# Kernel optimization log

Measured on AMD Instinct MI355X. Metric: run time of the kernel, lower is better.

## Reference

```python
import jax, jax.numpy as jnp
import numpy as np

H = W = 256
CX = CY = 128
N_RINGS = 16
RING_W = 8


def _ring_indices():
    """Static per-ring pixel coordinate lists (cv2 filled-circle rasterization
    approximated by Euclidean distance: ring i = { inner_r < dist <= outer_r }).
    Ring 0 excludes the exact center pixel, matching cv2.circle(radius=0) erase."""
    yy, xx = np.mgrid[0:H, 0:W]
    dist = np.sqrt((xx - CX) ** 2 + (yy - CY) ** 2)
    rings = []
    for i in range(N_RINGS):
        m = (dist <= (i + 1) * RING_W) & (dist > i * RING_W)
        ys, xs = np.nonzero(m)
        rings.append((jnp.asarray(ys), jnp.asarray(xs)))
    return rings

_RINGS = _ring_indices()


def setup_inputs() -> dict:
    key = jax.random.key(0)
    # normalized image in [0,1) so denorm->uint8 quantization never wraps
    image_tensor = jax.random.uniform(key, (256, 3, 256, 256), dtype=jnp.float32)
    return {"image_tensor": image_tensor}


def reference(image_tensor):
    # denormalize and quantize exactly like (img*0.5+0.5)*255 -> uint8 (truncation)
    img = jnp.floor((image_tensor * 0.5 + 0.5) * 255.0)  # [B,3,H,W], values 0..255
    feats = []
    for ys, xs in _RINGS:  # fixed 16-iteration structural loop
        px = img[:, :, ys, xs]                # [B, 3, N_ring] gather
        mean = jnp.mean(px, axis=-1)          # [B, 3]
        std = jnp.std(px, axis=-1)            # population std (ddof=0) like np
        med = jnp.median(px, axis=-1)         # [B, 3]
        feats.append(jnp.concatenate([mean, std, med], axis=-1))  # [B, 9]
    return jnp.stack(feats, axis=1)  # [B, 16, 9]
```

## Files before the change

kernel.cpp:

```cpp
#include <hip/hip_runtime.h>

#define IH 256
#define IW 256
#define NRINGS 16
#define LUT_WORDS (IH * IW / 4)

__global__ __launch_bounds__(256)
void k_ringlut(unsigned int* __restrict__ lut) {
    const int gid = blockIdx.x * 256 + threadIdx.x;
    const int y   = gid >> 6;
    const int x0  = (gid & 63) * 4;
    const int dy  = y - 128;
    const int dy2 = dy * dy;
    unsigned int w = 0;
    #pragma unroll
    for (int j = 0; j < 4; ++j) {
        const int dx = x0 + j - 128;
        const int d2 = dy2 + dx * dx;
        unsigned int r;
        if (d2 == 0 || d2 > 16384) r = 255u;
        else {
            int kk = (int)ceilf(sqrtf((float)d2) * 0.125f);
            if (64 * kk * kk < d2) kk++;
            else if (kk > 1 && 64 * (kk - 1) * (kk - 1) >= d2) kk--;
            r = (unsigned)(kk - 1);
        }
        w |= r << (8 * j);
    }
    lut[gid] = w;
}

__global__ __launch_bounds__(1024)
void radial_fused(const float* __restrict__ img,
                  const unsigned int* __restrict__ lut,
                  float* __restrict__ out) {
    const int b   = blockIdx.x;
    const int tid = threadIdx.x;

    __shared__ unsigned int hist[NRINGS * 3 * 256];

    for (int i = tid; i < NRINGS * 3 * 256; i += 1024) hist[i] = 0u;
    __syncthreads();

    const int xg = (tid & 63) * 4;
    const int r0 = tid >> 6;
    const float* base = img + (size_t)b * 3 * IH * IW;
    const int lc = xg >> 2;

    unsigned int rw[16];
    #pragma unroll
    for (int k = 0; k < 16; ++k) {
        const int y = r0 + (k << 4);
        rw[k] = lut[(y << 6) + lc];
    }

    #pragma unroll
    for (int k = 0; k < 16; ++k) {
        if (rw[k] == 0xFFFFFFFFu) continue;
        const int y   = r0 + (k << 4);
        const int off = y * IW + xg;
        const float4 f0 = *(const float4*)(base + off);
        const float4 f1 = *(const float4*)(base + IH * IW + off);
        const float4 f2 = *(const float4*)(base + 2 * IH * IW + off);
        const float va[3][4] = {{f0.x, f0.y, f0.z, f0.w},
                                {f1.x, f1.y, f1.z, f1.w},
                                {f2.x, f2.y, f2.z, f2.w}};

        #pragma unroll
        for (int j = 0; j < 4; ++j) {
            const unsigned int ring = (rw[k] >> (8 * j)) & 255u;
            if (ring == 255u) continue;
            unsigned int* hb = &hist[(ring * 3) << 8];
            #pragma unroll
            for (int c = 0; c < 3; ++c) {
                const float f = va[c][j];
                const int iv = (int)floorf((f * 0.5f + 0.5f) * 255.0f);
                atomicAdd(&hb[(c << 8) + iv], 1u);
            }
        }
    }

    __syncthreads();

    if (tid < NRINGS * 3) {
        const int ring = tid / 3;
        const int c    = tid - ring * 3;
        const unsigned int* h = &hist[((ring * 3 + c) << 8)];

        unsigned int n = 0, sum = 0, sumsq = 0;
        #pragma unroll 8
        for (int v = 0; v < 256; ++v) {
            const unsigned int cnt = h[v];
            n     += cnt;
            sum   += cnt * (unsigned)v;
            sumsq += cnt * (unsigned)(v * v);
        }

        const double dn   = (double)n;
        const double mean = (double)sum / dn;
        double var = (double)sumsq / dn - mean * mean;
        if (var < 0.0) var = 0.0;

        const unsigned int j1 = (n - 1u) >> 1;
        const unsigned int j2 = n >> 1;
        unsigned int cum = 0;
        int v1i = -1, v2i = -1;
        for (int v = 0; v < 256; ++v) {
            cum += h[v];
            if (v1i < 0 && cum > j1) v1i = v;
            if (cum > j2) { v2i = v; break; }
        }

        float* o = out + ((size_t)b * NRINGS + ring) * 9;
        o[c]     = (float)mean;
        o[3 + c] = (float)sqrt(var);
        o[6 + c] = 0.5f * (float)(v1i + v2i);
    }
}

extern "C" void kernel_launch(void* const* d_in, const int* in_sizes, int n_in,
                              void* d_out, int out_size, void* d_ws, size_t ws_size,
                              hipStream_t stream) {
    const float* img = (const float*)d_in[0];
    float* out = (float*)d_out;
    unsigned int* lut = (unsigned int*)d_ws;
    k_ringlut<<<LUT_WORDS / 256, 256, 0, stream>>>(lut);
    radial_fused<<<256, 1024, 0, stream>>>(img, lut, out);
}
```

Before: 288.0 us.

## Split per-image histogram across two blocks with global partial merge kernel

Splits each image's rows between two blocks that each build a shared-memory histogram and write it to workspace. A second kernel sums the two partials and computes mean, std and median. This doubles the number of blocks to raise GPU occupancy and parallelism. In exchange it adds a large global write and read of partial histograms and an extra launch. It also no longer skips rows that lie fully outside the rings.

```diff
diff --git a/kernel.cpp b/kernel.cpp
--- a/kernel.cpp
+++ b/kernel.cpp
@@ -3,7 +3,10 @@
 #define IH 256
 #define IW 256
 #define NRINGS 16
+#define NBINS (NRINGS * 3 * 256)
 #define LUT_WORDS (IH * IW / 4)
+#define LUT_BYTES ((size_t)LUT_WORDS * 4)
+#define PART_BYTES ((size_t)512 * NBINS * 4)
 
 __global__ __launch_bounds__(256)
 void k_ringlut(unsigned int* __restrict__ lut) {
@@ -31,41 +34,37 @@
 }
 
 __global__ __launch_bounds__(1024)
-void radial_fused(const float* __restrict__ img,
-                  const unsigned int* __restrict__ lut,
-                  float* __restrict__ out) {
-    const int b   = blockIdx.x;
-    const int tid = threadIdx.x;
-
-    __shared__ unsigned int hist[NRINGS * 3 * 256];
-
-    for (int i = tid; i < NRINGS * 3 * 256; i += 1024) hist[i] = 0u;
+void k1_hist(const float* __restrict__ img,
+             const unsigned int* __restrict__ lut,
+             unsigned int* __restrict__ parts) {
+    const int b    = blockIdx.x;
+    const int half = blockIdx.y;
+    const int tid  = threadIdx.x;
+
+    __shared__ __align__(16) unsigned int hist[NBINS];
+
+    for (int i = tid; i < NBINS; i += 1024) hist[i] = 0u;
     __syncthreads();
 
     const int xg = (tid & 63) * 4;
-    const int r0 = tid >> 6;
+    const int wv = tid >> 6;
+    const int y0 = (half << 7) + wv;
     const float* base = img + (size_t)b * 3 * IH * IW;
     const int lc = xg >> 2;
 
-    unsigned int rw[16];
-    #pragma unroll
-    for (int k = 0; k < 16; ++k) {
-        const int y = r0 + (k << 4);
-        rw[k] = lut[(y << 6) + lc];
-    }
-
-    #pragma unroll
-    for (int k = 0; k < 16; ++k) {
-        if (rw[k] == 0xFFFFFFFFu) continue;
-        const int y   = r0 + (k << 4);
-        const int off = y * IW + xg;
+    unsigned int rw[8];
+    #pragma unroll
+    for (int k = 0; k < 8; ++k) rw[k] = lut[((y0 + (k << 4)) << 6) + lc];
+
+    #pragma unroll
+    for (int k = 0; k < 8; ++k) {
+        const int off = (y0 + (k << 4)) * IW + xg;
         const float4 f0 = *(const float4*)(base + off);
         const float4 f1 = *(const float4*)(base + IH * IW + off);
         const float4 f2 = *(const float4*)(base + 2 * IH * IW + off);
         const float va[3][4] = {{f0.x, f0.y, f0.z, f0.w},
                                 {f1.x, f1.y, f1.z, f1.w},
                                 {f2.x, f2.y, f2.z, f2.w}};
-
         #pragma unroll
         for (int j = 0; j < 4; ++j) {
             const unsigned int ring = (rw[k] >> (8 * j)) & 255u;
@@ -73,19 +72,39 @@
             unsigned int* hb = &hist[(ring * 3) << 8];
             #pragma unroll
             for (int c = 0; c < 3; ++c) {
-                const float f = va[c][j];
-                const int iv = (int)floorf((f * 0.5f + 0.5f) * 255.0f);
+                const int iv = (int)floorf((va[c][j] * 0.5f + 0.5f) * 255.0f);
                 atomicAdd(&hb[(c << 8) + iv], 1u);
             }
         }
     }
 
+    __syncthreads();
+    uint4* dst = (uint4*)(parts + ((size_t)((b << 1) + half)) * NBINS);
+    const uint4* src = (const uint4*)hist;
+    #pragma unroll
+    for (int i = tid; i < NBINS / 4; i += 1024) dst[i] = src[i];
+}
+
+__global__ __launch_bounds__(1024)
+void k2_stats(const unsigned int* __restrict__ parts, float* __restrict__ out) {
+    const int b   = blockIdx.x;
+    const int tid = threadIdx.x;
+
+    __shared__ __align__(16) unsigned int hist[NBINS];
+
+    const uint4* p0 = (const uint4*)(parts + ((size_t)(b << 1)) * NBINS);
+    const uint4* p1 = (const uint4*)(parts + ((size_t)((b << 1) + 1)) * NBINS);
+    uint4* s = (uint4*)hist;
+    for (int i = tid; i < NBINS / 4; i += 1024) {
+        const uint4 a = p0[i], c = p1[i];
+        s[i] = make_uint4(a.x + c.x, a.y + c.y, a.z + c.z, a.w + c.w);
+    }
     __syncthreads();
 
     if (tid < NRINGS * 3) {
         const int ring = tid / 3;
         const int c    = tid - ring * 3;
-        const unsigned int* h = &hist[((ring * 3 + c) << 8)];
+        const unsigned int* h = &hist[tid << 8];
 
         unsigned int n = 0, sum = 0, sumsq = 0;
         #pragma unroll 8
@@ -114,6 +133,70 @@
         float* o = out + ((size_t)b * NRINGS + ring) * 9;
         o[c]     = (float)mean;
         o[3 + c] = (float)sqrt(var);
+        o[6 + c] = 0.5f * (float)(v1i + v2i);
+    }
+}
+
+__global__ __launch_bounds__(1024)
+void radial_fused(const float* __restrict__ img,
+                  const unsigned int* __restrict__ lut,
+                  float* __restrict__ out) {
+    const int b   = blockIdx.x;
+    const int tid = threadIdx.x;
+    __shared__ unsigned int hist[NBINS];
+    for (int i = tid; i < NBINS; i += 1024) hist[i] = 0u;
+    __syncthreads();
+    const int xg = (tid & 63) * 4;
+    const int r0 = tid >> 6;
+    const float* base = img + (size_t)b * 3 * IH * IW;
+    const int lc = xg >> 2;
+    unsigned int rw[16];
+    #pragma unroll
+    for (int k = 0; k < 16; ++k) rw[k] = lut[((r0 + (k << 4)) << 6) + lc];
+    #pragma unroll
+    for (int k = 0; k < 16; ++k) {
+        const int off = (r0 + (k << 4)) * IW + xg;
+        const float4 f0 = *(const float4*)(base + off);
+        const float4 f1 = *(const float4*)(base + IH * IW + off);
+        const float4 f2 = *(const float4*)(base + 2 * IH * IW + off);
+        const float va[3][4] = {{f0.x, f0.y, f0.z, f0.w},
+                                {f1.x, f1.y, f1.z, f1.w},
+                                {f2.x, f2.y, f2.z, f2.w}};
+        #pragma unroll
+        for (int j = 0; j < 4; ++j) {
+            const unsigned int ring = (rw[k] >> (8 * j)) & 255u;
+            if (ring == 255u) continue;
+            unsigned int* hb = &hist[(ring * 3) << 8];
+            #pragma unroll
+            for (int c = 0; c < 3; ++c) {
+                const int iv = (int)floorf((va[c][j] * 0.5f + 0.5f) * 255.0f);
+                atomicAdd(&hb[(c << 8) + iv], 1u);
+            }
+        }
+    }
+    __syncthreads();
+    if (tid < NRINGS * 3) {
+        const int ring = tid / 3;
+        const int c    = tid - ring * 3;
+        const unsigned int* h = &hist[tid << 8];
+        unsigned int n = 0, sum = 0, sumsq = 0;
+        for (int v = 0; v < 256; ++v) {
+            const unsigned int cnt = h[v];
+            n += cnt; sum += cnt * (unsigned)v; sumsq += cnt * (unsigned)(v * v);
+        }
+        const double dn = (double)n;
+        const double mean = (double)sum / dn;
+        double var = (double)sumsq / dn - mean * mean;
+        if (var < 0.0) var = 0.0;
+        const unsigned int j1 = (n - 1u) >> 1, j2 = n >> 1;
+        unsigned int cum = 0; int v1i = -1, v2i = -1;
+        for (int v = 0; v < 256; ++v) {
+            cum += h[v];
+            if (v1i < 0 && cum > j1) v1i = v;
+            if (cum > j2) { v2i = v; break; }
+        }
+        float* o = out + ((size_t)b * NRINGS + ring) * 9;
+        o[c] = (float)mean; o[3 + c] = (float)sqrt(var);
         o[6 + c] = 0.5f * (float)(v1i + v2i);
     }
 }
@@ -125,5 +208,11 @@
     float* out = (float*)d_out;
     unsigned int* lut = (unsigned int*)d_ws;
     k_ringlut<<<LUT_WORDS / 256, 256, 0, stream>>>(lut);
-    radial_fused<<<256, 1024, 0, stream>>>(img, lut, out);
-}
+    if (ws_size >= LUT_BYTES + PART_BYTES) {
+        unsigned int* parts = (unsigned int*)((char*)d_ws + LUT_BYTES);
+        k1_hist<<<dim3(256, 2), 1024, 0, stream>>>(img, lut, parts);
+        k2_stats<<<256, 1024, 0, stream>>>(parts, out);
+    } else {
+        radial_fused<<<256, 1024, 0, stream>>>(img, lut, out);
+    }
+}
```

Result: slower. 302.6 us (+5.1%).
